# Kernel tuning notes

Measured on AMD Instinct MI355X. Metric: run time of the kernel, lower is better.

Reference implementation:

```python
import jax, jax.numpy as jnp
import numpy as np


def _adj(M):
    # conjugate transpose of the last two (color) dims
    return jnp.conj(jnp.swapaxes(M, -1, -2))


def _plaquettes(U):
    # U: (B, L1..Ld, d, Nc, Nc) complex -> (B, L1..Ld, d*(d-1)/2, Nc, Nc)
    d = U.shape[-3]
    plaqs = []
    for mu in range(d):
        for nu in range(mu + 1, d):
            U_mu = U[..., mu, :, :]
            U_nu = U[..., nu, :, :]
            U_mu_fwd = jnp.roll(U_mu, -1, axis=1 + nu)
            U_nu_fwd = jnp.roll(U_nu, -1, axis=1 + mu)
            plaqs.append(U_mu @ U_nu_fwd @ _adj(U_mu_fwd) @ _adj(U_nu))
    return jnp.stack(plaqs, axis=-3)


def _polyakov(U):
    # Poly[..., mu] = U_mu(x) @ U_mu(x+mu) @ ... @ U_mu(x+(L_mu-1)mu)
    d = U.shape[-3]
    lattice_shape = U.shape[1:-3]
    loops = []
    for mu in range(d):
        U_mu = U[..., mu, :, :]
        P = U_mu
        shifted = U_mu
        for _ in range(1, lattice_shape[mu]):
            shifted = jnp.roll(shifted, -1, axis=1 + mu)
            P = P @ shifted
        loops.append(P)
    return jnp.stack(loops, axis=-3)


def setup_inputs() -> dict:
    key = jax.random.key(0)
    ks = jax.random.split(key, 4)
    B, L, d, Nc = 2, 16, 4, 3
    N_out, N_in, K = 8, 10, 1
    shapeU = (B, L, L, L, L, d, Nc, Nc)
    return {
        "U_re": jax.random.normal(ks[0], shapeU, jnp.float32),
        "U_im": jax.random.normal(ks[1], shapeU, jnp.float32),
        "omega_re": jax.random.normal(ks[2], (N_out, N_in, d, 2 * K + 1), jnp.float32),
        "omega_im": jax.random.normal(ks[3], (N_out, N_in, d, 2 * K + 1), jnp.float32),
        "K": K,
        "N_out": N_out,
    }


def reference(U_re, U_im, omega_re, omega_im, K, N_out):
    U = U_re + 1j * U_im            # complex64 gauge links (B, L1..L4, d, Nc, Nc)
    omega = omega_re + 1j * omega_im  # (N_out, N_in, d, 2K+1)
    d = U.shape[-3]

    # W = locally transforming variables: plaquettes + Polyakov loops, N_in channels
    W = jnp.concatenate([_plaquettes(U), _polyakov(U)], axis=-3)

    # NOTE: the original torch get_ParallelTransporters never writes the cumulative
    # products back into the tensor (in-place bug), so the transporters used by
    # L_conv are exactly U_mu for every shift k. We reproduce that behavior.
    W_conv = jnp.zeros(U.shape[:-3] + (N_out,) + U.shape[-2:], dtype=U.dtype)
    for k in range(-K, K + 1):
        i_k = k + K
        for mu in range(d):
            W_sh = jnp.roll(W, -k, axis=1 + mu)      # (B, lat, N_in, Nc, Nc)
            A = U[..., mu, :, :]                      # effective transporter (B, lat, Nc, Nc)
            W_conv = W_conv + jnp.einsum(
                'ij,...ac,...jcd,...db->...iab',
                omega[..., mu, i_k], A, W_sh, _adj(A), optimize=True)
    return W_conv
```

## Files before the change

kernel.cpp:

```cpp
#include <hip/hip_runtime.h>

#define LSZ   16
#define NBATCH 2
#define NSITE (NBATCH*LSZ*LSZ*LSZ*LSZ)
#define NIN   10
#define NOUT  8
#define ND    4
#define NCPLX ((long)NSITE * NOUT * 9)
#define NLINE_PER_DIR (NSITE / LSZ)
#define NLINK (NSITE * ND)
#define WSTRIDE 108

typedef unsigned int u32;
typedef float  f32x4 __attribute__((ext_vector_type(4)));
typedef short  s16x8 __attribute__((ext_vector_type(8)));
typedef float  f32x4a __attribute__((ext_vector_type(4), aligned(4)));

struct M3 { float re[9]; float im[9]; };

__device__ __forceinline__ void load9(float d[9], const float* __restrict__ p) {
    f32x4a a = *reinterpret_cast<const f32x4a*>(p);
    f32x4a b = *reinterpret_cast<const f32x4a*>(p + 4);
    d[0] = a[0]; d[1] = a[1]; d[2] = a[2]; d[3] = a[3];
    d[4] = b[0]; d[5] = b[1]; d[6] = b[2]; d[7] = b[3];
    d[8] = p[8];
}

__device__ __forceinline__ unsigned short f2bf(float x) {
    u32 u = __float_as_uint(x);
    u32 r = (u + 0x7fffu + ((u >> 16) & 1u)) >> 16;
    return (unsigned short)r;
}
__device__ __forceinline__ u32 packbf(float lo, float hi) {
    return (u32)f2bf(lo) | ((u32)f2bf(hi) << 16);
}

__device__ __forceinline__ s16x8 as_s16x8(uint4 v) {
    union { uint4 u; s16x8 s; } x; x.u = v; return x.s;
}

__device__ __forceinline__ void mulM(M3& o, const M3& a, const M3& b) {
#pragma unroll
    for (int r = 0; r < 3; r++) {
#pragma unroll
        for (int c = 0; c < 3; c++) {
            float xr = 0.f, xi = 0.f;
#pragma unroll
            for (int k = 0; k < 3; k++) {
                float ar = a.re[r*3+k], ai = a.im[r*3+k];
                float br = b.re[k*3+c], bi = b.im[k*3+c];
                xr = fmaf(ar, br, xr); xr = fmaf(-ai, bi, xr);
                xi = fmaf(ar, bi, xi); xi = fmaf(ai, br, xi);
            }
            o.re[r*3+c] = xr; o.im[r*3+c] = xi;
        }
    }
}

__device__ __forceinline__ void mulAdjM(M3& o, const M3& a, const M3& b) {
#pragma unroll
    for (int r = 0; r < 3; r++) {
#pragma unroll
        for (int c = 0; c < 3; c++) {
            float xr = 0.f, xi = 0.f;
#pragma unroll
            for (int k = 0; k < 3; k++) {
                float ar = a.re[r*3+k], ai = a.im[r*3+k];
                float br = b.re[c*3+k], bi = b.im[c*3+k];
                xr = fmaf(ar, br, xr); xr = fmaf(ai, bi, xr);
                xi = fmaf(ai, br, xi); xi = fmaf(-ar, bi, xi);
            }
            o.re[r*3+c] = xr; o.im[r*3+c] = xi;
        }
    }
}

__device__ __forceinline__ int shift_site(int s, int mu, int k) {
    int sh = 12 - 4 * mu;
    int c  = (s >> sh) & 15;
    int nc = (c + k) & 15;
    return (s & ~(15 << sh)) | (nc << sh);
}

__global__ __launch_bounds__(256) void poly_kernel(const float* __restrict__ Ure,
                                                   const float* __restrict__ Uim,
                                                   u32* __restrict__ T2) {
    __shared__ float2 sm[16 * 145];

    int line0 = blockIdx.x * 16;
    int mu    = line0 / NLINE_PER_DIR;
    int lidx0 = line0 - mu * NLINE_PER_DIR;
    int sh    = 12 - 4 * mu;
    int low0  = lidx0 & ((1 << sh) - 1);
    int high0 = lidx0 >> sh;
    int s_base0 = (high0 << (sh + 4)) | low0;

    for (int n = threadIdx.x; n < 16 * 16 * 9; n += 256) {
        int siteIdx = n / 9;
        int e       = n - siteIdx * 9;
        int site, l, c;
        if (mu == 3) { site = (lidx0 << 4) + siteIdx; l = siteIdx >> 4; c = siteIdx & 15; }
        else         { site = s_base0 + ((siteIdx >> 4) << sh) + (siteIdx & 15);
                       l = siteIdx & 15; c = siteIdx >> 4; }
        long g = ((long)site * 4 + mu) * 9 + e;
        sm[l * 145 + c * 9 + e] = make_float2(Ure[g], Uim[g]);
    }
    __syncthreads();

    int lane = threadIdx.x & 63;
    int c    = threadIdx.x & 15;
    int l    = threadIdx.x >> 4;

    M3 P;
    {
        const float2* m0 = &sm[l * 145 + c * 9];
#pragma unroll
        for (int e = 0; e < 9; e++) { float2 v = m0[e]; P.re[e] = v.x; P.im[e] = v.y; }
    }

#pragma unroll
    for (int k = 1; k < 16; k <<= 1) {
        int src = (lane & 48) | ((c + k) & 15);
        M3 Q, T;
#pragma unroll
        for (int e = 0; e < 9; e++) {
            Q.re[e] = __shfl(P.re[e], src);
            Q.im[e] = __shfl(P.im[e], src);
        }
        mulM(T, P, Q);
        P = T;
    }

    int lidx = lidx0 + l;
    int low  = lidx & ((1 << sh) - 1);
    int high = lidx >> sh;
    int site = (high << (sh + 4)) | (c << sh) | low;
    u32* Tp = T2 + ((long)site * 4 + mu) * 9;
#pragma unroll
    for (int e = 0; e < 9; e++) Tp[e] = packbf(P.re[e], P.im[e]);
}

__global__ __launch_bounds__(192) void plaq_merge_kernel(const float* __restrict__ Ure,
                                                         const float* __restrict__ Uim,
                                                         const u32* __restrict__ T2,
                                                         u32* __restrict__ W) {
    __shared__ u32 sw[32 * WSTRIDE];

    int s0 = blockIdx.x * 32;

    u32 tpre[6]; int tofs[6];
#pragma unroll
    for (int w = 0; w < 6; w++) {
        int it = threadIdx.x + w * 192;
        tpre[w] = T2[(long)s0 * 36 + it];
        int ls2 = it / 36;
        int r   = it - ls2 * 36;
        int mu2 = r / 9;
        int e2  = r - mu2 * 9;
        tofs[w] = ls2 * WSTRIDE + e2 * 12 + 6 + mu2;
    }

    int p  = threadIdx.x >> 5;
    int ls = threadIdx.x & 31;
    int s  = s0 + ls;

    int mu = (p < 3) ? 0 : ((p < 5) ? 1 : 2);
    int nu = (mu == 0) ? (p + 1) : ((mu == 1) ? (p - 1) : 3);

    M3 Umu, Unu, Unu_f, Umu_f, T1, T2m, P;
#define LDG(m, site, link) { \
        long base_ = ((long)(site) * 4 + (link)) * 9; \
        load9((m).re, Ure + base_); \
        load9((m).im, Uim + base_); }

    LDG(Umu,   s,                      mu);
    LDG(Unu,   s,                      nu);
    LDG(Unu_f, shift_site(s, mu, 1),   nu);
    LDG(Umu_f, shift_site(s, nu, 1),   mu);
#undef LDG

    mulM(T1, Umu, Unu_f);
    mulAdjM(T2m, T1, Umu_f);
    mulAdjM(P, T2m, Unu);

#pragma unroll
    for (int e = 0; e < 9; e++) sw[ls * WSTRIDE + e * 12 + p] = packbf(P.re[e], P.im[e]);

    for (int it = threadIdx.x; it < 32 * 9 * 2; it += 192) {
        int site = it / 18;
        int r    = it - site * 18;
        sw[site * WSTRIDE + (r >> 1) * 12 + 10 + (r & 1)] = 0u;
    }

#pragma unroll
    for (int w = 0; w < 6; w++) sw[tofs[w]] = tpre[w];
    __syncthreads();

    uint4* W4 = (uint4*)W;
    for (int it = threadIdx.x; it < 27 * 32; it += 192) {
        int pl  = it >> 5;
        int ls2 = it & 31;
        int e   = pl / 3, q = pl - e * 3;
        const uint4 v = *(const uint4*)(sw + ls2 * WSTRIDE + e * 12 + q * 4);
        W4[(long)pl * NSITE + s0 + ls2] = v;
    }
}

template <int MODE>
__global__ __launch_bounds__(256) void conv_kernel(const float* __restrict__ Ure,
                                                   const float* __restrict__ Uim,
                                                   const u32* __restrict__ W,
                                                   const float* __restrict__ omre,
                                                   const float* __restrict__ omim,
                                                   float* __restrict__ out) {
    __shared__ __align__(16) char smraw[64 * 72 * sizeof(float)];
    uint4* somB = (uint4*)smraw;
    float* sout = (float*)smraw;

    for (int n = threadIdx.x; n < 12 * 64; n += 256) {
        int mk = n >> 6, ln = n & 63;
        int q = ln >> 4, c = ln & 15, i = c & 7;
        int mu = mk / 3, kk = mk - mu * 3;
        u32 wv[4];
#pragma unroll
        for (int w = 0; w < 4; w++) {
            int j = q * 4 + w;
            u32 val = 0u;
            if (q < 3 && j < NIN) {
                int oidx = ((i * NIN + j) * ND + mu) * 3 + kk;
                float orv = omre[oidx], oiv = omim[oidx];
                val = (c < 8) ? packbf(orv, -oiv) : packbf(oiv, orv);
            }
            wv[w] = val;
        }
        somB[n] = make_uint4(wv[0], wv[1], wv[2], wv[3]);
    }
    __syncthreads();

    int chunk = gridDim.x >> 3;
    int lb    = ((int)blockIdx.x & 7) * chunk + ((int)blockIdx.x >> 3);

    int lane = threadIdx.x & 63;
    int wv_  = threadIdx.x >> 6;
    int r    = lane & 15;
    int q    = lane >> 4;
    int s0b  = lb * 64;
    int sline = s0b + wv_ * 16;

    const uint4* W4 = (const uint4*)W;

    bool hi = (r >= 8);
    int  i  = r & 7;
    int  reg0 = hi ? 2 : 0;

    float accr[2][9], acci[2][9];
#pragma unroll
    for (int rr = 0; rr < 2; rr++)
#pragma unroll
        for (int e = 0; e < 9; e++) { accr[rr][e] = 0.f; acci[rr][e] = 0.f; }

    for (int mu = 0; mu < ND; mu++) {
        f32x4 acc[9];
#pragma unroll
        for (int e = 0; e < 9; e++) acc[e] = (f32x4)(0.f);

        for (int kk = 0; kk < 3; kk++) {
            int mk = mu * 3 + kk;
            s16x8 bfrag = as_s16x8(somB[mk * 64 + lane]);

            int nb;
            if (mu < 3) nb = shift_site(sline, mu, kk - 1) + r;
            else        nb = sline + ((r + kk - 1) & 15);

            uint4 w9[9];
            if (q < 3) {
#pragma unroll
                for (int e = 0; e < 9; e++) w9[e] = W4[(long)(e * 3 + q) * NSITE + nb];
            } else {
#pragma unroll
                for (int e = 0; e < 9; e++) w9[e] = make_uint4(0u, 0u, 0u, 0u);
            }
#pragma unroll
            for (int e = 0; e < 9; e++)
                acc[e] = __builtin_amdgcn_mfma_f32_16x16x32_bf16(as_s16x8(w9[e]), bfrag, acc[e], 0, 0, 0);
        }

        float own[2][9], oth[2][9];
#pragma unroll
        for (int e = 0; e < 9; e++) {
            float t0 = __shfl_xor(acc[e][0], 8);
            float t1 = __shfl_xor(acc[e][1], 8);
            float t2 = __shfl_xor(acc[e][2], 8);
            float t3 = __shfl_xor(acc[e][3], 8);
            own[0][e] = hi ? acc[e][2] : acc[e][0];
            own[1][e] = hi ? acc[e][3] : acc[e][1];
            oth[0][e] = hi ? t2 : t0;
            oth[1][e] = hi ? t3 : t1;
        }

#pragma unroll
        for (int rr = 0; rr < 2; rr++) {
            int site = sline + q * 4 + reg0 + rr;
            M3 A, M;
            {
                long base_ = ((long)site * 4 + mu) * 9;
                load9(A.re, Ure + base_);
                load9(A.im, Uim + base_);
            }
#pragma unroll
            for (int e = 0; e < 9; e++) {
                M.re[e] = hi ? oth[rr][e] : own[rr][e];
                M.im[e] = hi ? own[rr][e] : oth[rr][e];
            }
            M3 Tm;
#pragma unroll
            for (int rw = 0; rw < 3; rw++) {
#pragma unroll
                for (int cl = 0; cl < 3; cl++) {
                    float xr = 0.f, xi = 0.f;
#pragma unroll
                    for (int k = 0; k < 3; k++) {
                        float ar = A.re[rw*3+k], ai = A.im[rw*3+k];
                        float br = M.re[k*3+cl], bi = M.im[k*3+cl];
                        xr = fmaf(ar, br, xr); xr = fmaf(-ai, bi, xr);
                        xi = fmaf(ar, bi, xi); xi = fmaf(ai, br, xi);
                    }
                    Tm.re[rw*3+cl] = xr; Tm.im[rw*3+cl] = xi;
                }
            }
#pragma unroll
            for (int rw = 0; rw < 3; rw++) {
#pragma unroll
                for (int cl = 0; cl < 3; cl++) {
                    float xr = 0.f, xi = 0.f;
#pragma unroll
                    for (int k = 0; k < 3; k++) {
                        float ar = Tm.re[rw*3+k], ai = Tm.im[rw*3+k];
                        float br = A.re[cl*3+k], bi = A.im[cl*3+k];
                        xr = fmaf(ar, br, xr); xr = fmaf(ai, bi, xr);
                        if (MODE != 2) { xi = fmaf(ai, br, xi); xi = fmaf(-ar, bi, xi); }
                    }
                    accr[rr][rw*3+cl] += xr;
                    if (MODE != 2) acci[rr][rw*3+cl] += xi;
                }
            }
        }
    }

    if (MODE == 2) {
        __syncthreads();
#pragma unroll
        for (int rr = 0; rr < 2; rr++) {
            int tloc = wv_ * 16 + q * 4 + reg0 + rr;
#pragma unroll
            for (int e = 0; e < 9; e++)
                sout[(tloc * 8 + i) * 9 + e] = accr[rr][e];
        }
        __syncthreads();
        float4*       o4 = (float4*)(out + (long)lb * 4608);
        const float4* s4 = (const float4*)sout;
        for (int n = threadIdx.x; n < 1152; n += 256) o4[n] = s4[n];
    } else if (MODE == 0) {
#pragma unroll
        for (int rr = 0; rr < 2; rr++) {
            int site = sline + q * 4 + reg0 + rr;
            long cb = ((long)site * 8 + i) * 9;
            float2* op = (float2*)(out + cb * 2);
#pragma unroll
            for (int e = 0; e < 9; e++) op[e] = make_float2(accr[rr][e], acci[rr][e]);
        }
    } else {
#pragma unroll
        for (int rr = 0; rr < 2; rr++) {
            int site = sline + q * 4 + reg0 + rr;
            long cb = ((long)site * 8 + i) * 9;
#pragma unroll
            for (int e = 0; e < 9; e++) {
                out[cb + e]         = accr[rr][e];
                out[NCPLX + cb + e] = acci[rr][e];
            }
        }
    }
}

extern "C" void kernel_launch(void* const* d_in, const int* in_sizes, int n_in,
                              void* d_out, int out_size, void* d_ws, size_t ws_size,
                              hipStream_t stream) {
    const float* Ure  = (const float*)d_in[0];
    const float* Uim  = (const float*)d_in[1];
    const float* omre = (const float*)d_in[2];
    const float* omim = (const float*)d_in[3];
    float* out = (float*)d_out;

    const size_t wBytes = (size_t)NSITE * WSTRIDE * sizeof(u32);
    if (ws_size < wBytes) return;

    u32* W  = (u32*)d_ws;
    u32* T2 = (u32*)d_out;

    poly_kernel<<<NSITE * 4 / (16 * 16), 256, 0, stream>>>(Ure, Uim, T2);
    plaq_merge_kernel<<<NSITE / 32, 192, 0, stream>>>(Ure, Uim, T2, W);

    const int convGrid = NSITE / 64;
    if (out_size == (int)NCPLX)
        conv_kernel<2><<<convGrid, 256, 0, stream>>>(Ure, Uim, W, omre, omim, out);
    else if (out_size == (int)(2 * NCPLX))
        conv_kernel<1><<<convGrid, 256, 0, stream>>>(Ure, Uim, W, omre, omim, out);
    else
        conv_kernel<0><<<convGrid, 256, 0, stream>>>(Ure, Uim, W, omre, omim, out);
}
```

Before: 218.7 us.

## Write U links in plane-major float2 layout from poly kernel for plaquette loads

poly_kernel, which already stages each link line in shared memory, now also writes the links to a workspace buffer in a structure-of-arrays layout (link, element, site) with interleaved re/im pairs. plaq_merge_kernel then reads from this buffer, so adjacent threads make coalesced float2 loads instead of strided, unaligned 9-float AoS loads from the separate re/im arrays. The cost is an extra write of the full U field (about 18 MB) in poly_kernel and a larger workspace requirement, which returns early if too small.

```diff
diff --git a/kernel.cpp b/kernel.cpp
--- a/kernel.cpp
+++ b/kernel.cpp
@@ -84,7 +84,8 @@
 
 __global__ __launch_bounds__(256) void poly_kernel(const float* __restrict__ Ure,
                                                    const float* __restrict__ Uim,
-                                                   u32* __restrict__ T2) {
+                                                   u32* __restrict__ T2,
+                                                   float2* __restrict__ Uplane) {
     __shared__ float2 sm[16 * 145];
 
     int line0 = blockIdx.x * 16;
@@ -107,6 +108,21 @@
     }
     __syncthreads();
 
+    for (int n = threadIdx.x; n < 9 * 256; n += 256) {
+        int e   = n >> 8;
+        int idx = n & 255;
+        int l, c, site;
+        if (mu == 3) { site = (lidx0 << 4) + idx; l = idx >> 4; c = idx & 15; }
+        else {
+            c = idx >> 4; l = idx & 15;
+            int lidx = lidx0 + l;
+            int low  = lidx & ((1 << sh) - 1);
+            int high = lidx >> sh;
+            site = (high << (sh + 4)) | (c << sh) | low;
+        }
+        Uplane[(long)(mu * 9 + e) * NSITE + site] = sm[l * 145 + c * 9 + e];
+    }
+
     int lane = threadIdx.x & 63;
     int c    = threadIdx.x & 15;
     int l    = threadIdx.x >> 4;
@@ -140,8 +156,7 @@
     for (int e = 0; e < 9; e++) Tp[e] = packbf(P.re[e], P.im[e]);
 }
 
-__global__ __launch_bounds__(192) void plaq_merge_kernel(const float* __restrict__ Ure,
-                                                         const float* __restrict__ Uim,
+__global__ __launch_bounds__(192) void plaq_merge_kernel(const float2* __restrict__ Uplane,
                                                          const u32* __restrict__ T2,
                                                          u32* __restrict__ W) {
     __shared__ u32 sw[32 * WSTRIDE];
@@ -168,16 +183,16 @@
     int nu = (mu == 0) ? (p + 1) : ((mu == 1) ? (p - 1) : 3);
 
     M3 Umu, Unu, Unu_f, Umu_f, T1, T2m, P;
-#define LDG(m, site, link) { \
-        long base_ = ((long)(site) * 4 + (link)) * 9; \
-        load9((m).re, Ure + base_); \
-        load9((m).im, Uim + base_); }
-
-    LDG(Umu,   s,                      mu);
-    LDG(Unu,   s,                      nu);
-    LDG(Unu_f, shift_site(s, mu, 1),   nu);
-    LDG(Umu_f, shift_site(s, nu, 1),   mu);
-#undef LDG
+#define LDP(m, site_, link_) { \
+        const float2* pp = Uplane + (long)(link_) * 9 * NSITE + (site_); \
+        _Pragma("unroll") \
+        for (int e = 0; e < 9; e++) { float2 v = pp[(long)e * NSITE]; (m).re[e] = v.x; (m).im[e] = v.y; } }
+
+    LDP(Umu,   s,                      mu);
+    LDP(Unu,   s,                      nu);
+    LDP(Unu_f, shift_site(s, mu, 1),   nu);
+    LDP(Umu_f, shift_site(s, nu, 1),   mu);
+#undef LDP
 
     mulM(T1, Umu, Unu_f);
     mulAdjM(T2m, T1, Umu_f);
@@ -392,14 +407,16 @@
     const float* omim = (const float*)d_in[3];
     float* out = (float*)d_out;
 
-    const size_t wBytes = (size_t)NSITE * WSTRIDE * sizeof(u32);
-    if (ws_size < wBytes) return;
-
-    u32* W  = (u32*)d_ws;
-    u32* T2 = (u32*)d_out;
-
-    poly_kernel<<<NSITE * 4 / (16 * 16), 256, 0, stream>>>(Ure, Uim, T2);
-    plaq_merge_kernel<<<NSITE / 32, 192, 0, stream>>>(Ure, Uim, T2, W);
+    const size_t wBytes  = (size_t)NSITE * WSTRIDE * sizeof(u32);
+    const size_t upBytes = (size_t)36 * NSITE * sizeof(float2);
+    if (ws_size < wBytes + upBytes) return;
+
+    u32*    W      = (u32*)d_ws;
+    float2* Uplane = (float2*)((char*)d_ws + wBytes);
+    u32*    T2     = (u32*)d_out;
+
+    poly_kernel<<<NSITE * 4 / (16 * 16), 256, 0, stream>>>(Ure, Uim, T2, Uplane);
+    plaq_merge_kernel<<<NSITE / 32, 192, 0, stream>>>(Uplane, T2, W);
 
     const int convGrid = NSITE / 64;
     if (out_size == (int)NCPLX)
```

Measured after the change: 208.3 us. -4.8%, faster.
